# Kernel tuning notes

Hardware: AMD Instinct MI355X
Metric: run time of the kernel (lower is better)

The kernel has to match this reference:

```python
import jax, jax.numpy as jnp
import numpy as np

B, H, L, DH = 4, 16, 2048, 64
EMBED_DIM = H * DH
CAUSAL = True


def setup_inputs() -> dict:
    key = jax.random.key(0)
    kq, kk, kv = jax.random.split(key, 3)
    return {
        "query": jax.random.normal(kq, (B, H, L, DH), dtype=jnp.float32),
        "key": jax.random.normal(kk, (B, H, L, DH), dtype=jnp.float32),
        "value": jax.random.normal(kv, (B, H, L, DH), dtype=jnp.float32),
    }


def reference(query, key, value):
    # scaled dot-product attention with causal mask, inputs [B, H, L, Dh]
    scale = 1.0 / jnp.sqrt(jnp.asarray(query.shape[-1], query.dtype))
    scores = jnp.einsum("bhld,bhsd->bhls", query, key) * scale  # [B,H,L,S]
    if CAUSAL:
        q_idx = jnp.arange(query.shape[-2])[:, None]
        k_idx = jnp.arange(key.shape[-2])[None, :]
        neg_inf = jnp.asarray(-jnp.inf, scores.dtype)
        scores = jnp.where(k_idx > q_idx, neg_inf, scores)
    attn = jax.nn.softmax(scores, axis=-1)
    out = jnp.einsum("bhls,bhsd->bhld", attn, value)  # [B,H,L,Dh]
    # merge heads -> [B, L, D]
    b = out.shape[0]
    return out.transpose(0, 2, 1, 3).reshape(b, -1, EMBED_DIM)
```

## Files before the change

### kernel.cpp

```cpp
#include <hip/hip_runtime.h>
#include <hip/hip_bf16.h>

#define B_   4
#define H_   16
#define L_   2048
#define DH_  64
#define QSCALE 0.1803368801111204f
#define LDK  72

typedef __bf16 bf16;
typedef __bf16 bf16x4 __attribute__((ext_vector_type(4)));
typedef __bf16 bf16x8 __attribute__((ext_vector_type(8)));
typedef float  f32x4  __attribute__((ext_vector_type(4)));

typedef const __attribute__((address_space(1))) unsigned int* gptr_t;
typedef __attribute__((address_space(3))) unsigned int* lptr_t;

__device__ __forceinline__ void load_lds16(const bf16* g, bf16* l) {
    __builtin_amdgcn_global_load_lds((gptr_t)(const void*)g, (lptr_t)(void*)l, 16, 0, 0);
}

__global__ __launch_bounds__(256, 4)
void prep(const float* __restrict__ K, const float* __restrict__ V,
          bf16* __restrict__ Kb, bf16* __restrict__ Vtg)
{
    __shared__ bf16 tl[64 * 72];
    const int t   = threadIdx.x;
    const int r   = t >> 2;
    const int c4  = t & 3;
    const int bid = blockIdx.x;
    const int kt  = bid & 31;
    const int bh  = bid >> 5;

    const float* Kp = K + ((size_t)bh * L_ + kt * 64) * DH_;
    const float* Vp = V + ((size_t)bh * L_ + kt * 64) * DH_;
    bf16* Kbp = Kb  + (size_t)bh * (L_ * DH_) + (size_t)(kt * 64) * DH_;
    bf16* Vtp = Vtg + (size_t)bh * (DH_ * L_) + kt * 64;

    {
        const float* src = Kp + r * DH_ + c4 * 16;
        f32x4 a = *(const f32x4*)(src);
        f32x4 b = *(const f32x4*)(src + 4);
        f32x4 c = *(const f32x4*)(src + 8);
        f32x4 d = *(const f32x4*)(src + 12);
        bf16x8 lo, hi;
        #pragma unroll
        for (int j = 0; j < 4; ++j) {
            lo[j] = (bf16)a[j]; lo[j + 4] = (bf16)b[j];
            hi[j] = (bf16)c[j]; hi[j + 4] = (bf16)d[j];
        }
        const int b0 = 2 * c4, b1 = 2 * c4 + 1;
        *(bf16x8*)(Kbp + r * 64 + (b0 ^ (r & 7)) * 8) = lo;
        *(bf16x8*)(Kbp + r * 64 + (b1 ^ (r & 7)) * 8) = hi;
    }
    {
        const float* src = Vp + r * DH_ + c4 * 16;
        f32x4 a = *(const f32x4*)(src);
        f32x4 b = *(const f32x4*)(src + 4);
        f32x4 c = *(const f32x4*)(src + 8);
        f32x4 d = *(const f32x4*)(src + 12);
        #pragma unroll
        for (int j = 0; j < 4; ++j) {
            tl[(c4 * 16 + j)      * 72 + r] = (bf16)a[j];
            tl[(c4 * 16 + 4 + j)  * 72 + r] = (bf16)b[j];
            tl[(c4 * 16 + 8 + j)  * 72 + r] = (bf16)c[j];
            tl[(c4 * 16 + 12 + j) * 72 + r] = (bf16)d[j];
        }
    }
    __syncthreads();
    {
        const int d = r;
        #pragma unroll
        for (int bi = 0; bi < 2; ++bi) {
            const int blk = 2 * c4 + bi;
            bf16x8 v;
            #pragma unroll
            for (int j = 0; j < 8; ++j) v[j] = tl[d * 72 + blk * 8 + j];
            *(bf16x8*)(Vtp + (size_t)d * L_ + (blk ^ (d & 7)) * 8) = v;
        }
    }
}

__global__ __launch_bounds__(256, 2)
void fa_fwd3(const float* __restrict__ Q, const bf16* __restrict__ Kb,
             const bf16* __restrict__ Vtg, float* __restrict__ O)
{
    __shared__ __align__(16) bf16 smem[2][2][64 * 64];
    __shared__ __align__(16) bf16 Pl[4][16 * 64];

    const int tid  = threadIdx.x;
    const int wave = tid >> 6;
    const int lane = tid & 63;
    const int quad = lane >> 4;
    const int l15  = lane & 15;

    const int u    = blockIdx.x;
    const int xcd  = u & 7;
    const int t    = u >> 3;
    const int bh   = xcd * 8 + (t & 7);
    const int pidx = t >> 3;

    const int h    = bh & 15;
    const int b    = bh >> 4;

    const float* Qbh = Q + (size_t)bh * L_ * DH_;
    const bf16* Kbh  = Kb  + (size_t)bh * (L_ * DH_);
    const bf16* Vbh  = Vtg + (size_t)bh * (DH_ * L_);

    const int Rw = 16 * wave;
    const int lr = lane >> 3;
    const int lb = lane & 7;

    bf16x8 vone;
    #pragma unroll
    for (int jj = 0; jj < 8; ++jj) vone[jj] = (bf16)1.0f;

    int swb[2];
    #pragma unroll
    for (int s = 0; s < 2; ++s) swb[s] = ((4 * s + quad) ^ (l15 & 7)) * 8;

    for (int pass = 0; pass < 2; ++pass) {
        const int Qt  = pass ? (15 - pidx) : pidx;
        const int q0  = Qt * 128;
        const int jmax = 2 * Qt + 1;

        bf16x8 qf[2][2];
        #pragma unroll
        for (int qg = 0; qg < 2; ++qg) {
            const int row = q0 + 32 * wave + 16 * qg + l15;
            const float* qp = Qbh + (size_t)row * DH_ + quad * 8;
            #pragma unroll
            for (int s = 0; s < 2; ++s) {
                f32x4 a = *(const f32x4*)(qp + s * 32);
                f32x4 c = *(const f32x4*)(qp + s * 32 + 4);
                #pragma unroll
                for (int jj = 0; jj < 4; ++jj) {
                    qf[qg][s][jj]     = (bf16)(a[jj] * QSCALE);
                    qf[qg][s][jj + 4] = (bf16)(c[jj] * QSCALE);
                }
            }
        }

        f32x4 o_acc[2][4];
        f32x4 l_acc[2];
        #pragma unroll
        for (int qg = 0; qg < 2; ++qg) {
            l_acc[qg] = (f32x4)0.0f;
            #pragma unroll
            for (int ct = 0; ct < 4; ++ct) o_acc[qg][ct] = (f32x4)0.0f;
        }

        {
            const bf16* kg = Kbh + (size_t)(Rw + lr) * 64 + lb * 8;
            const bf16* vg = Vbh + (size_t)(Rw + lr) * L_ + lb * 8;
            bf16* kl = &smem[0][0][Rw * 64];
            bf16* vl = &smem[0][1][Rw * 64];
            load_lds16(kg, kl);              load_lds16(kg + 8 * 64, kl + 8 * 64);
            load_lds16(vg, vl);              load_lds16(vg + (size_t)8 * L_, vl + 8 * 64);
        }

        for (int j = 0; j <= jmax; ++j) {
            __syncthreads();
            const int cur = j & 1;

            if (j < jmax) {
                const int nb  = cur ^ 1;
                const int kv0 = (j + 1) * 64;
                const bf16* kg = Kbh + (size_t)(kv0 + Rw + lr) * 64 + lb * 8;
                const bf16* vg = Vbh + (size_t)(Rw + lr) * L_ + kv0 + lb * 8;
                bf16* kl = &smem[nb][0][Rw * 64];
                bf16* vl = &smem[nb][1][Rw * 64];
                load_lds16(kg, kl);          load_lds16(kg + 8 * 64, kl + 8 * 64);
                load_lds16(vg, vl);          load_lds16(vg + (size_t)8 * L_, vl + 8 * 64);
            }

            const bf16* Kl = smem[cur][0];
            const bf16* Vt = smem[cur][1];

            bf16x8 bk[4][2];
            #pragma unroll
            for (int ct = 0; ct < 4; ++ct)
                #pragma unroll
                for (int s = 0; s < 2; ++s)
                    bk[ct][s] = *(const bf16x8*)&Kl[(16 * ct + l15) * 64 + swb[s]];

            bf16x8 pa[2][2];
            #pragma unroll
            for (int qg = 0; qg < 2; ++qg) {
                f32x4 sacc[4];
                #pragma unroll
                for (int ct = 0; ct < 4; ++ct) {
                    f32x4 acc = (f32x4)0.0f;
                    #pragma unroll
                    for (int s = 0; s < 2; ++s)
                        acc = __builtin_amdgcn_mfma_f32_16x16x32_bf16(bk[ct][s], qf[qg][s], acc, 0, 0, 0);
                    sacc[ct] = acc;
                }

                if (j >= 2 * Qt) {
                    const int rlim = 32 * wave + 16 * qg + l15 - ((j - 2 * Qt) << 6);
                    #pragma unroll
                    for (int ct = 0; ct < 4; ++ct) {
                        #pragma unroll
                        for (int r = 0; r < 4; ++r)
                            if (16 * ct + quad * 4 + r > rlim) sacc[ct][r] = -1e30f;
                    }
                }

                #pragma unroll
                for (int ct = 0; ct < 4; ++ct) {
                    bf16x4 pk;
                    #pragma unroll
                    for (int r = 0; r < 4; ++r) pk[r] = (bf16)exp2f(sacc[ct][r]);
                    const int blk = 2 * ct + (quad >> 1);
                    *(bf16x4*)&Pl[wave][l15 * 64 + ((blk ^ (l15 & 7)) * 8) + (quad & 1) * 4] = pk;
                }
                #pragma unroll
                for (int s = 0; s < 2; ++s)
                    pa[qg][s] = *(const bf16x8*)&Pl[wave][l15 * 64 + swb[s]];
            }

            #pragma unroll
            for (int ct = 0; ct < 4; ++ct) {
                #pragma unroll
                for (int s = 0; s < 2; ++s) {
                    bf16x8 bv = *(const bf16x8*)&Vt[(16 * ct + l15) * 64 + swb[s]];
                    #pragma unroll
                    for (int qg = 0; qg < 2; ++qg)
                        o_acc[qg][ct] = __builtin_amdgcn_mfma_f32_16x16x32_bf16(pa[qg][s], bv, o_acc[qg][ct], 0, 0, 0);
                }
            }
            #pragma unroll
            for (int qg = 0; qg < 2; ++qg)
                #pragma unroll
                for (int s = 0; s < 2; ++s)
                    l_acc[qg] = __builtin_amdgcn_mfma_f32_16x16x32_bf16(pa[qg][s], vone, l_acc[qg], 0, 0, 0);
        }
        __syncthreads();

        #pragma unroll
        for (int qg = 0; qg < 2; ++qg)
            #pragma unroll
            for (int r = 0; r < 4; ++r) {
                const float inv = 1.0f / l_acc[qg][r];
                const int qrow = q0 + 32 * wave + 16 * qg + quad * 4 + r;
                float* op = &O[((size_t)b * L_ + qrow) * (H_ * DH_) + h * DH_];
                #pragma unroll
                for (int ct = 0; ct < 4; ++ct)
                    op[16 * ct + l15] = o_acc[qg][ct][r] * inv;
            }
    }
}

__global__ __launch_bounds__(256, 4)
void fa_fwd(const float* __restrict__ Q, const float* __restrict__ K,
            const float* __restrict__ V, float* __restrict__ O)
{
    __shared__ __align__(16) bf16 Kl[64 * LDK];
    __shared__ __align__(16) bf16 Vt[64 * LDK];
    __shared__ __align__(16) bf16 Pl[4][16 * LDK];

    const int tid  = threadIdx.x;
    const int wave = tid >> 6;
    const int lane = tid & 63;
    const int quad = lane >> 4;
    const int l15  = lane & 15;

    const int u    = blockIdx.x;
    const int xcd  = u & 7;
    const int p    = u >> 3;
    const int bh   = xcd * 8 + (p & 7);
    const int pidx = p >> 3;
    const int h    = bh & 15;
    const int b    = bh >> 4;

    const float* Qbh = Q + (size_t)bh * L_ * DH_;
    const float* Kbh = K + (size_t)bh * L_ * DH_;
    const float* Vbh = V + (size_t)bh * L_ * DH_;

    const int r0 = tid >> 4;
    const int c0 = (tid & 15) * 4;

    for (int pass = 0; pass < 2; ++pass) {
        const int qt = pass ? (31 - pidx) : pidx;
        const int q0 = qt * 64;

        bf16x8 qf[2];
        {
            const int row = q0 + wave * 16 + l15;
            const float* qp = Qbh + (size_t)row * DH_ + quad * 8;
            #pragma unroll
            for (int s = 0; s < 2; ++s) {
                f32x4 a = *(const f32x4*)(qp + s * 32);
                f32x4 c = *(const f32x4*)(qp + s * 32 + 4);
                #pragma unroll
                for (int jj = 0; jj < 4; ++jj) {
                    qf[s][jj]     = (bf16)(a[jj] * QSCALE);
                    qf[s][jj + 4] = (bf16)(c[jj] * QSCALE);
                }
            }
        }

        float m_run[4], l_run[4];
        f32x4 o_acc[4];
        #pragma unroll
        for (int r = 0; r < 4; ++r) { m_run[r] = -1e30f; l_run[r] = 0.0f; }
        #pragma unroll
        for (int ct = 0; ct < 4; ++ct) o_acc[ct] = (f32x4)0.0f;

        f32x4 kreg[4], vreg[4];
        #pragma unroll
        for (int i = 0; i < 4; ++i) {
            kreg[i] = *(const f32x4*)(Kbh + (size_t)(r0 + 16 * i) * DH_ + c0);
            vreg[i] = *(const f32x4*)(Vbh + (size_t)(r0 + 16 * i) * DH_ + c0);
        }

        for (int j = 0; j <= qt; ++j) {
            __syncthreads();
            #pragma unroll
            for (int i = 0; i < 4; ++i) {
                const int row = r0 + 16 * i;
                bf16x4 kb;
                #pragma unroll
                for (int c = 0; c < 4; ++c) kb[c] = (bf16)kreg[i][c];
                *(bf16x4*)&Kl[row * LDK + c0] = kb;
                Vt[(c0 + 0) * LDK + row] = (bf16)vreg[i][0];
                Vt[(c0 + 1) * LDK + row] = (bf16)vreg[i][1];
                Vt[(c0 + 2) * LDK + row] = (bf16)vreg[i][2];
                Vt[(c0 + 3) * LDK + row] = (bf16)vreg[i][3];
            }
            __syncthreads();

            if (j < qt) {
                const int kv0 = (j + 1) * 64;
                #pragma unroll
                for (int i = 0; i < 4; ++i) {
                    kreg[i] = *(const f32x4*)(Kbh + (size_t)(kv0 + r0 + 16 * i) * DH_ + c0);
                    vreg[i] = *(const f32x4*)(Vbh + (size_t)(kv0 + r0 + 16 * i) * DH_ + c0);
                }
            }

            f32x4 sacc[4];
            #pragma unroll
            for (int ct = 0; ct < 4; ++ct) {
                f32x4 acc = (f32x4)0.0f;
                #pragma unroll
                for (int s = 0; s < 2; ++s) {
                    bf16x8 bk = *(const bf16x8*)&Kl[(16 * ct + l15) * LDK + 32 * s + quad * 8];
                    acc = __builtin_amdgcn_mfma_f32_16x16x32_bf16(qf[s], bk, acc, 0, 0, 0);
                }
                sacc[ct] = acc;
            }

            if (j == qt) {
                #pragma unroll
                for (int ct = 0; ct < 4; ++ct) {
                    const int keyl = 16 * ct + l15;
                    #pragma unroll
                    for (int r = 0; r < 4; ++r)
                        if (keyl > wave * 16 + quad * 4 + r) sacc[ct][r] = -1e30f;
                }
            }

            #pragma unroll
            for (int r = 0; r < 4; ++r) {
                float mx = fmaxf(fmaxf(sacc[0][r], sacc[1][r]), fmaxf(sacc[2][r], sacc[3][r]));
                mx = fmaxf(mx, __shfl_xor(mx, 1));
                mx = fmaxf(mx, __shfl_xor(mx, 2));
                mx = fmaxf(mx, __shfl_xor(mx, 4));
                mx = fmaxf(mx, __shfl_xor(mx, 8));
                const float mnew  = fmaxf(m_run[r], mx);
                const float alpha = exp2f(m_run[r] - mnew);
                float sum = 0.0f;
                #pragma unroll
                for (int ct = 0; ct < 4; ++ct) {
                    const float pv = exp2f(sacc[ct][r] - mnew);
                    sacc[ct][r] = pv;
                    sum += pv;
                }
                sum += __shfl_xor(sum, 1);
                sum += __shfl_xor(sum, 2);
                sum += __shfl_xor(sum, 4);
                sum += __shfl_xor(sum, 8);
                l_run[r] = l_run[r] * alpha + sum;
                m_run[r] = mnew;
                #pragma unroll
                for (int ct = 0; ct < 4; ++ct) o_acc[ct][r] *= alpha;
            }

            #pragma unroll
            for (int ct = 0; ct < 4; ++ct)
                #pragma unroll
                for (int r = 0; r < 4; ++r)
                    Pl[wave][(quad * 4 + r) * LDK + 16 * ct + l15] = (bf16)sacc[ct][r];

            bf16x8 pa[2];
            #pragma unroll
            for (int s = 0; s < 2; ++s)
                pa[s] = *(const bf16x8*)&Pl[wave][l15 * LDK + 32 * s + quad * 8];

            #pragma unroll
            for (int ct = 0; ct < 4; ++ct)
                #pragma unroll
                for (int s = 0; s < 2; ++s) {
                    bf16x8 bv = *(const bf16x8*)&Vt[(16 * ct + l15) * LDK + 32 * s + quad * 8];
                    o_acc[ct] = __builtin_amdgcn_mfma_f32_16x16x32_bf16(pa[s], bv, o_acc[ct], 0, 0, 0);
                }
        }

        #pragma unroll
        for (int ct = 0; ct < 4; ++ct)
            #pragma unroll
            for (int r = 0; r < 4; ++r) {
                const int qrow = q0 + wave * 16 + quad * 4 + r;
                O[((size_t)b * L_ + qrow) * (H_ * DH_) + h * DH_ + (16 * ct + l15)] =
                    o_acc[ct][r] / l_run[r];
            }
    }
}

extern "C" void kernel_launch(void* const* d_in, const int* in_sizes, int n_in,
                              void* d_out, int out_size, void* d_ws, size_t ws_size,
                              hipStream_t stream) {
    const float* q = (const float*)d_in[0];
    const float* k = (const float*)d_in[1];
    const float* v = (const float*)d_in[2];
    float* out = (float*)d_out;
    const size_t need = 2ull * (size_t)(B_ * H_) * L_ * DH_ * sizeof(bf16);
    if (ws_size >= need) {
        bf16* Kb  = (bf16*)d_ws;
        bf16* Vtg = Kb + (size_t)(B_ * H_) * L_ * DH_;
        prep<<<dim3(B_ * H_ * (L_ / 64)), dim3(256), 0, stream>>>(k, v, Kb, Vtg);
        fa_fwd3<<<dim3(512), dim3(256), 0, stream>>>(q, Kb, Vtg, out);
    } else {
        fa_fwd<<<dim3(B_ * H_ * 16), dim3(256), 0, stream>>>(q, k, v, out);
    }
}
```

Baseline: 190.4 us.

## Split paired causal passes into separate blocks and skip fully-masked wave tiles

Each block previously handled two 128-row query tiles in sequence (a short one and a long one) to balance causal work. Now each block handles one tile, the grid doubles to 1024 blocks, and a new index mapping interleaves long and short tiles so heavy blocks are dispatched first. Launch bounds rise to 4 blocks per CU, and waves whose query rows are fully masked for the current diagonal KV block skip their MFMA work. This aims at better occupancy and load balance but gives up the per-block pairing balance and may add register pressure under the tighter launch bound.

```diff
diff --git a/kernel.cpp b/kernel.cpp
--- a/kernel.cpp
+++ b/kernel.cpp
@@ -81,7 +81,7 @@
     }
 }
 
-__global__ __launch_bounds__(256, 2)
+__global__ __launch_bounds__(256, 4)
 void fa_fwd3(const float* __restrict__ Q, const bf16* __restrict__ Kb,
              const bf16* __restrict__ Vtg, float* __restrict__ O)
 {
@@ -95,10 +95,12 @@
     const int l15  = lane & 15;
 
     const int u    = blockIdx.x;
-    const int xcd  = u & 7;
-    const int t    = u >> 3;
-    const int bh   = xcd * 8 + (t & 7);
-    const int pidx = t >> 3;
+    const int bh   = u & 63;
+    const int s    = u >> 6;
+    const int kq   = s >> 2;
+    const int s0   = s & 3;
+    const int base = ((kq & 1) == 0) ? (15 - (kq >> 1)) : (kq >> 1);
+    const int Qt   = (kq & 1) ? (base + 2 * s0) : (base - 2 * s0);
 
     const int h    = bh & 15;
     const int b    = bh >> 4;
@@ -117,63 +119,63 @@
 
     int swb[2];
     #pragma unroll
-    for (int s = 0; s < 2; ++s) swb[s] = ((4 * s + quad) ^ (l15 & 7)) * 8;
-
-    for (int pass = 0; pass < 2; ++pass) {
-        const int Qt  = pass ? (15 - pidx) : pidx;
-        const int q0  = Qt * 128;
-        const int jmax = 2 * Qt + 1;
-
-        bf16x8 qf[2][2];
-        #pragma unroll
-        for (int qg = 0; qg < 2; ++qg) {
-            const int row = q0 + 32 * wave + 16 * qg + l15;
-            const float* qp = Qbh + (size_t)row * DH_ + quad * 8;
-            #pragma unroll
-            for (int s = 0; s < 2; ++s) {
-                f32x4 a = *(const f32x4*)(qp + s * 32);
-                f32x4 c = *(const f32x4*)(qp + s * 32 + 4);
-                #pragma unroll
-                for (int jj = 0; jj < 4; ++jj) {
-                    qf[qg][s][jj]     = (bf16)(a[jj] * QSCALE);
-                    qf[qg][s][jj + 4] = (bf16)(c[jj] * QSCALE);
-                }
-            }
-        }
-
-        f32x4 o_acc[2][4];
-        f32x4 l_acc[2];
-        #pragma unroll
-        for (int qg = 0; qg < 2; ++qg) {
-            l_acc[qg] = (f32x4)0.0f;
-            #pragma unroll
-            for (int ct = 0; ct < 4; ++ct) o_acc[qg][ct] = (f32x4)0.0f;
-        }
-
-        {
-            const bf16* kg = Kbh + (size_t)(Rw + lr) * 64 + lb * 8;
-            const bf16* vg = Vbh + (size_t)(Rw + lr) * L_ + lb * 8;
-            bf16* kl = &smem[0][0][Rw * 64];
-            bf16* vl = &smem[0][1][Rw * 64];
-            load_lds16(kg, kl);              load_lds16(kg + 8 * 64, kl + 8 * 64);
-            load_lds16(vg, vl);              load_lds16(vg + (size_t)8 * L_, vl + 8 * 64);
-        }
-
-        for (int j = 0; j <= jmax; ++j) {
-            __syncthreads();
-            const int cur = j & 1;
-
-            if (j < jmax) {
-                const int nb  = cur ^ 1;
-                const int kv0 = (j + 1) * 64;
-                const bf16* kg = Kbh + (size_t)(kv0 + Rw + lr) * 64 + lb * 8;
-                const bf16* vg = Vbh + (size_t)(Rw + lr) * L_ + kv0 + lb * 8;
-                bf16* kl = &smem[nb][0][Rw * 64];
-                bf16* vl = &smem[nb][1][Rw * 64];
-                load_lds16(kg, kl);          load_lds16(kg + 8 * 64, kl + 8 * 64);
-                load_lds16(vg, vl);          load_lds16(vg + (size_t)8 * L_, vl + 8 * 64);
-            }
-
+    for (int ss = 0; ss < 2; ++ss) swb[ss] = ((4 * ss + quad) ^ (l15 & 7)) * 8;
+
+    const int q0   = Qt * 128;
+    const int jmax = 2 * Qt + 1;
+
+    bf16x8 qf[2][2];
+    #pragma unroll
+    for (int qg = 0; qg < 2; ++qg) {
+        const int row = q0 + 32 * wave + 16 * qg + l15;
+        const float* qp = Qbh + (size_t)row * DH_ + quad * 8;
+        #pragma unroll
+        for (int ss = 0; ss < 2; ++ss) {
+            f32x4 a = *(const f32x4*)(qp + ss * 32);
+            f32x4 c = *(const f32x4*)(qp + ss * 32 + 4);
+            #pragma unroll
+            for (int jj = 0; jj < 4; ++jj) {
+                qf[qg][ss][jj]     = (bf16)(a[jj] * QSCALE);
+                qf[qg][ss][jj + 4] = (bf16)(c[jj] * QSCALE);
+            }
+        }
+    }
+
+    f32x4 o_acc[2][4];
+    f32x4 l_acc[2];
+    #pragma unroll
+    for (int qg = 0; qg < 2; ++qg) {
+        l_acc[qg] = (f32x4)0.0f;
+        #pragma unroll
+        for (int ct = 0; ct < 4; ++ct) o_acc[qg][ct] = (f32x4)0.0f;
+    }
+
+    {
+        const bf16* kg = Kbh + (size_t)(Rw + lr) * 64 + lb * 8;
+        const bf16* vg = Vbh + (size_t)(Rw + lr) * L_ + lb * 8;
+        bf16* kl = &smem[0][0][Rw * 64];
+        bf16* vl = &smem[0][1][Rw * 64];
+        load_lds16(kg, kl);              load_lds16(kg + 8 * 64, kl + 8 * 64);
+        load_lds16(vg, vl);              load_lds16(vg + (size_t)8 * L_, vl + 8 * 64);
+    }
+
+    for (int j = 0; j <= jmax; ++j) {
+        __syncthreads();
+        const int cur = j & 1;
+
+        if (j < jmax) {
+            const int nb  = cur ^ 1;
+            const int kv0 = (j + 1) * 64;
+            const bf16* kg = Kbh + (size_t)(kv0 + Rw + lr) * 64 + lb * 8;
+            const bf16* vg = Vbh + (size_t)(Rw + lr) * L_ + kv0 + lb * 8;
+            bf16* kl = &smem[nb][0][Rw * 64];
+            bf16* vl = &smem[nb][1][Rw * 64];
+            load_lds16(kg, kl);          load_lds16(kg + 8 * 64, kl + 8 * 64);
+            load_lds16(vg, vl);          load_lds16(vg + (size_t)8 * L_, vl + 8 * 64);
+        }
+
+        const bool active = (j < 2 * Qt) || ((32 * wave + 31) >= ((j - 2 * Qt) << 6));
+        if (active) {
             const bf16* Kl = smem[cur][0];
             const bf16* Vt = smem[cur][1];
 
@@ -181,8 +183,8 @@
             #pragma unroll
             for (int ct = 0; ct < 4; ++ct)
                 #pragma unroll
-                for (int s = 0; s < 2; ++s)
-                    bk[ct][s] = *(const bf16x8*)&Kl[(16 * ct + l15) * 64 + swb[s]];
+                for (int ss = 0; ss < 2; ++ss)
+                    bk[ct][ss] = *(const bf16x8*)&Kl[(16 * ct + l15) * 64 + swb[ss]];
 
             bf16x8 pa[2][2];
             #pragma unroll
@@ -192,8 +194,8 @@
                 for (int ct = 0; ct < 4; ++ct) {
                     f32x4 acc = (f32x4)0.0f;
                     #pragma unroll
-                    for (int s = 0; s < 2; ++s)
-                        acc = __builtin_amdgcn_mfma_f32_16x16x32_bf16(bk[ct][s], qf[qg][s], acc, 0, 0, 0);
+                    for (int ss = 0; ss < 2; ++ss)
+                        acc = __builtin_amdgcn_mfma_f32_16x16x32_bf16(bk[ct][ss], qf[qg][ss], acc, 0, 0, 0);
                     sacc[ct] = acc;
                 }
 
@@ -216,40 +218,39 @@
                     *(bf16x4*)&Pl[wave][l15 * 64 + ((blk ^ (l15 & 7)) * 8) + (quad & 1) * 4] = pk;
                 }
                 #pragma unroll
-                for (int s = 0; s < 2; ++s)
-                    pa[qg][s] = *(const bf16x8*)&Pl[wave][l15 * 64 + swb[s]];
+                for (int ss = 0; ss < 2; ++ss)
+                    pa[qg][ss] = *(const bf16x8*)&Pl[wave][l15 * 64 + swb[ss]];
             }
 
             #pragma unroll
             for (int ct = 0; ct < 4; ++ct) {
                 #pragma unroll
-                for (int s = 0; s < 2; ++s) {
-                    bf16x8 bv = *(const bf16x8*)&Vt[(16 * ct + l15) * 64 + swb[s]];
+                for (int ss = 0; ss < 2; ++ss) {
+                    bf16x8 bv = *(const bf16x8*)&Vt[(16 * ct + l15) * 64 + swb[ss]];
                     #pragma unroll
                     for (int qg = 0; qg < 2; ++qg)
-                        o_acc[qg][ct] = __builtin_amdgcn_mfma_f32_16x16x32_bf16(pa[qg][s], bv, o_acc[qg][ct], 0, 0, 0);
+                        o_acc[qg][ct] = __builtin_amdgcn_mfma_f32_16x16x32_bf16(pa[qg][ss], bv, o_acc[qg][ct], 0, 0, 0);
                 }
             }
             #pragma unroll
             for (int qg = 0; qg < 2; ++qg)
                 #pragma unroll
-                for (int s = 0; s < 2; ++s)
-                    l_acc[qg] = __builtin_amdgcn_mfma_f32_16x16x32_bf16(pa[qg][s], vone, l_acc[qg], 0, 0, 0);
-        }
-        __syncthreads();
-
-        #pragma unroll
-        for (int qg = 0; qg < 2; ++qg)
-            #pragma unroll
-            for (int r = 0; r < 4; ++r) {
-                const float inv = 1.0f / l_acc[qg][r];
-                const int qrow = q0 + 32 * wave + 16 * qg + quad * 4 + r;
-                float* op = &O[((size_t)b * L_ + qrow) * (H_ * DH_) + h * DH_];
-                #pragma unroll
-                for (int ct = 0; ct < 4; ++ct)
-                    op[16 * ct + l15] = o_acc[qg][ct][r] * inv;
-            }
-    }
+                for (int ss = 0; ss < 2; ++ss)
+                    l_acc[qg] = __builtin_amdgcn_mfma_f32_16x16x32_bf16(pa[qg][ss], vone, l_acc[qg], 0, 0, 0);
+        }
+    }
+
+    #pragma unroll
+    for (int qg = 0; qg < 2; ++qg)
+        #pragma unroll
+        for (int r = 0; r < 4; ++r) {
+            const float inv = 1.0f / l_acc[qg][r];
+            const int qrow = q0 + 32 * wave + 16 * qg + quad * 4 + r;
+            float* op = &O[((size_t)b * L_ + qrow) * (H_ * DH_) + h * DH_];
+            #pragma unroll
+            for (int ct = 0; ct < 4; ++ct)
+                op[16 * ct + l15] = o_acc[qg][ct][r] * inv;
+        }
 }
 
 __global__ __launch_bounds__(256, 4)
@@ -431,7 +432,7 @@
         bf16* Kb  = (bf16*)d_ws;
         bf16* Vtg = Kb + (size_t)(B_ * H_) * L_ * DH_;
         prep<<<dim3(B_ * H_ * (L_ / 64)), dim3(256), 0, stream>>>(k, v, Kb, Vtg);
-        fa_fwd3<<<dim3(512), dim3(256), 0, stream>>>(q, Kb, Vtg, out);
+        fa_fwd3<<<dim3(1024), dim3(256), 0, stream>>>(q, Kb, Vtg, out);
     } else {
         fa_fwd<<<dim3(B_ * H_ * 16), dim3(256), 0, stream>>>(q, k, v, out);
     }
```

Result: slower. 194.6 us (+2.2%).
